# Performance work log

Hardware: AMD Instinct MI355X
Metric: run time of the kernel (lower is better)

## Reference

```python
import jax, jax.numpy as jnp
import numpy as np

DIM_VAL = 128
DIM_ATTN = 64

def setup_inputs() -> dict:
    key = jax.random.key(0)
    k_x, k_q, k_k, k_v = jax.random.split(key, 4)
    B, S = 4, 4096
    x = jax.random.normal(k_x, (B, S, DIM_VAL), dtype=jnp.float32)
    # nn.Linear(in, out, bias=False): weight shape [out, in]; y = x @ W^T
    Wq = jax.random.normal(k_q, (DIM_ATTN, DIM_VAL), dtype=jnp.float32) / np.sqrt(DIM_VAL)
    Wk = jax.random.normal(k_k, (DIM_ATTN, DIM_VAL), dtype=jnp.float32) / np.sqrt(DIM_VAL)
    Wv = jax.random.normal(k_v, (DIM_VAL, DIM_VAL), dtype=jnp.float32) / np.sqrt(DIM_VAL)
    return {"x": x, "Wq": Wq, "Wk": Wk, "Wv": Wv}

def reference(x, Wq, Wk, Wv):
    # QKV projections (bias-free linear: x @ W^T)
    Q = jnp.einsum('bsd,ad->bsa', x, Wq)   # [B,S,dim_attn]
    K = jnp.einsum('bsd,ad->bsa', x, Wk)   # [B,S,dim_attn]
    V = jnp.einsum('bsd,vd->bsv', x, Wv)   # [B,S,dim_val]
    scale = 1.0 / jnp.sqrt(jnp.asarray(Q.shape[-1], dtype=Q.dtype))
    scores = jnp.einsum('bqa,bka->bqk', Q, K) * scale  # [B,S,S]
    a = jax.nn.softmax(scores, axis=-1)
    return jnp.einsum('bqk,bkv->bqv', a, V)  # [B,S,dim_val]
```

## Files before the change

### kernel.cpp

```cpp
#include <hip/hip_runtime.h>

typedef _Float16 half8 __attribute__((ext_vector_type(8)));
typedef _Float16 half4v __attribute__((ext_vector_type(4)));
typedef float   float4v __attribute__((ext_vector_type(4)));

#define S_LEN 4096
#define NBATCH 4
#define NCHUNK 4
#define WS_W16 0
#define WS_QH  32768
#define WS_KH  1081344
#define WS_VT  2129920
#define WS_L   4227072
#define OACC_BYTE_OFF 8519680ull
#define OACC_F4_PER_CHUNK (NBATCH * S_LEN * 128 / 4)
#define LACC_BYTE_OFF (OACC_BYTE_OFF + (unsigned long long)NCHUNK * NBATCH * S_LEN * 128 * 4)
#define WS_NEED_BYTES (LACC_BYTE_OFF + (unsigned long long)NCHUNK * NBATCH * S_LEN * 4)

__global__ __launch_bounds__(256) void wcvt_kernel(const float* __restrict__ Wq,
                                                   const float* __restrict__ Wk,
                                                   const float* __restrict__ Wv,
                                                   _Float16* __restrict__ w16) {
    int i = blockIdx.x * 256 + threadIdx.x;
    int row = i >> 7, col = i & 127;
    float v;
    if (row < 64)       v = Wq[row * 128 + col];
    else if (row < 128) v = Wk[(row - 64) * 128 + col];
    else                v = Wv[(row - 128) * 128 + col];
    w16[i] = (_Float16)v;
}

__global__ __launch_bounds__(256) void zero_kernel(float4v* __restrict__ out4,
                                                   float4v* __restrict__ l4) {
    int i = blockIdx.x * 256 + threadIdx.x;
    out4[i] = (float4v){0.f, 0.f, 0.f, 0.f};
    if (i < 4096) l4[i] = (float4v){0.f, 0.f, 0.f, 0.f};
}

__global__ __launch_bounds__(256) void qkv_proj_kernel(const float* __restrict__ x,
                                                       const _Float16* __restrict__ w16,
                                                       _Float16* __restrict__ Qh,
                                                       _Float16* __restrict__ Kh,
                                                       _Float16* __restrict__ Vt) {
    __shared__ _Float16 xs[16 * 136];
    const int t = threadIdx.x;
    const int blk = blockIdx.x;
    const float* xb = x + (size_t)blk * 16 * 128;

    for (int it = 0; it < 2; ++it) {
        int i = t + it * 256;
        int row = i >> 5, c4 = i & 31;
        float4v f = ((const float4v*)xb)[i];
        half4v h;
        h[0] = (_Float16)f[0]; h[1] = (_Float16)f[1];
        h[2] = (_Float16)f[2]; h[3] = (_Float16)f[3];
        *(half4v*)&xs[row * 136 + c4 * 4] = h;
    }
    __syncthreads();

    const int w = t >> 6, lane = t & 63, quad = lane >> 4, n16 = lane & 15;

    half8 a[4];
    for (int c = 0; c < 4; ++c)
        a[c] = *(const half8*)&xs[n16 * 136 + c * 32 + quad * 8];

    float4v acc[4];
    for (int nb = 0; nb < 4; ++nb) acc[nb] = (float4v){0.f, 0.f, 0.f, 0.f};

    for (int c = 0; c < 4; ++c) {
        for (int nb = 0; nb < 4; ++nb) {
            int oc = w * 64 + nb * 16 + n16;
            half8 bfr = *(const half8*)&w16[(size_t)oc * 128 + c * 32 + quad * 8];
            acc[nb] = __builtin_amdgcn_mfma_f32_16x16x32_f16(a[c], bfr, acc[nb], 0, 0, 0);
        }
    }

    const int token0 = blk * 16 + quad * 4;
    if (w == 0) {
        for (int nb = 0; nb < 4; ++nb)
            for (int r = 0; r < 4; ++r)
                Qh[(size_t)(token0 + r) * 64 + nb * 16 + n16] = (_Float16)acc[nb][r];
    } else if (w == 1) {
        for (int nb = 0; nb < 4; ++nb)
            for (int r = 0; r < 4; ++r)
                Kh[(size_t)(token0 + r) * 64 + nb * 16 + n16] = (_Float16)acc[nb][r];
    } else {
        const int bb = token0 >> 12, s0 = token0 & 4095;
        const int kt = s0 >> 6, k0 = s0 & 63;
        const int grp = k0 >> 5, k32 = k0 & 31;
        const int g = k32 >> 4, q = (k32 >> 2) & 3;
        const int off = kt * 64 + grp * 32 + q * 8 + g * 4;
        for (int nb = 0; nb < 4; ++nb) {
            const int vc = (w - 2) * 64 + nb * 16 + n16;
            half4v h;
            h[0] = (_Float16)acc[nb][0]; h[1] = (_Float16)acc[nb][1];
            h[2] = (_Float16)acc[nb][2]; h[3] = (_Float16)acc[nb][3];
            *(half4v*)&Vt[((size_t)bb * 128 + vc) * S_LEN + off] = h;
        }
    }
}

#define KT 64
template <bool STAGED>
__global__ __launch_bounds__(256) void flash_kernel(const _Float16* __restrict__ Qh,
                                                    const _Float16* __restrict__ Kh,
                                                    const _Float16* __restrict__ Vt,
                                                    float* __restrict__ outp,
                                                    float* __restrict__ lp) {
    __shared__ _Float16 Ks[KT * 72];
    __shared__ _Float16 Vs[128 * 72];

    const int t = threadIdx.x;
    const int qt = blockIdx.x, chunk = blockIdx.y, b = blockIdx.z;
    const int w = t >> 6, lane = t & 63, quad = lane >> 4, n16 = lane & 15;

    const size_t qrowA = (size_t)b * S_LEN + qt * 128 + w * 16 + n16;
    const size_t qrowB = qrowA + 64;
    half8 aQ0A = *(const half8*)&Qh[qrowA * 64 + quad * 8];
    half8 aQ1A = *(const half8*)&Qh[qrowA * 64 + 32 + quad * 8];
    half8 aQ0B = *(const half8*)&Qh[qrowB * 64 + quad * 8];
    half8 aQ1B = *(const half8*)&Qh[qrowB * 64 + 32 + quad * 8];

    float4v OA[8], OB[8];
#pragma unroll
    for (int vb = 0; vb < 8; ++vb) {
        OA[vb] = (float4v){0.f, 0.f, 0.f, 0.f};
        OB[vb] = (float4v){0.f, 0.f, 0.f, 0.f};
    }
    float lsumA = 0.f, lsumB = 0.f;

    const _Float16* Kb = Kh + (size_t)b * S_LEN * 64;
    const _Float16* Vb = Vt + (size_t)b * 128 * S_LEN;

    const int kt0 = chunk * (S_LEN / KT / NCHUNK);
    const int kt1 = kt0 + (S_LEN / KT / NCHUNK);

    const int kr0 = t >> 3, kc0 = t & 7;
    const int kr1 = (t + 256) >> 3;

    half8 kreg0, kreg1, vreg[4];
    {
        const half8* srcK = (const half8*)(Kb + (size_t)kt0 * KT * 64);
        kreg0 = srcK[t];
        kreg1 = srcK[t + 256];
#pragma unroll
        for (int it = 0; it < 4; ++it) {
            int i = t + it * 256, row = i >> 3, c8 = i & 7;
            vreg[it] = *(const half8*)&Vb[(size_t)row * S_LEN + kt0 * KT + c8 * 8];
        }
    }

    for (int kt = kt0; kt < kt1; ++kt) {
        __syncthreads();
        *(half8*)&Ks[kr0 * 72 + kc0 * 8] = kreg0;
        *(half8*)&Ks[kr1 * 72 + kc0 * 8] = kreg1;
#pragma unroll
        for (int it = 0; it < 4; ++it) {
            int i = t + it * 256, row = i >> 3, c8 = i & 7;
            *(half8*)&Vs[row * 72 + c8 * 8] = vreg[it];
        }
        __syncthreads();

        if (kt + 1 < kt1) {
            const half8* srcK = (const half8*)(Kb + (size_t)(kt + 1) * KT * 64);
            kreg0 = srcK[t];
            kreg1 = srcK[t + 256];
#pragma unroll
            for (int it = 0; it < 4; ++it) {
                int i = t + it * 256, row = i >> 3, c8 = i & 7;
                vreg[it] = *(const half8*)&Vb[(size_t)row * S_LEN + (kt + 1) * KT + c8 * 8];
            }
        }

        half8 aP0A, aP1A, aP0B, aP1B;
        __builtin_amdgcn_s_setprio(1);
#pragma unroll
        for (int nb = 0; nb < 4; ++nb) {
            half8 bK0 = *(const half8*)&Ks[(nb * 16 + n16) * 72 + quad * 8];
            half8 bK1 = *(const half8*)&Ks[(nb * 16 + n16) * 72 + 32 + quad * 8];
            float4v scA = (float4v){0.f, 0.f, 0.f, 0.f};
            float4v scB = (float4v){0.f, 0.f, 0.f, 0.f};
            scA = __builtin_amdgcn_mfma_f32_16x16x32_f16(bK0, aQ0A, scA, 0, 0, 0);
            scA = __builtin_amdgcn_mfma_f32_16x16x32_f16(bK1, aQ1A, scA, 0, 0, 0);
            scB = __builtin_amdgcn_mfma_f32_16x16x32_f16(bK0, aQ0B, scB, 0, 0, 0);
            scB = __builtin_amdgcn_mfma_f32_16x16x32_f16(bK1, aQ1B, scB, 0, 0, 0);
#pragma unroll
            for (int r = 0; r < 4; ++r) {
                float pa = __builtin_amdgcn_exp2f(__builtin_fmaf(scA[r], 0.18033688f, -5.7707802f));
                lsumA += pa;
                float pb = __builtin_amdgcn_exp2f(__builtin_fmaf(scB[r], 0.18033688f, -5.7707802f));
                lsumB += pb;
                int slot = (nb & 1) * 4 + r;
                if (nb < 2) { aP0A[slot] = (_Float16)pa; aP0B[slot] = (_Float16)pb; }
                else        { aP1A[slot] = (_Float16)pa; aP1B[slot] = (_Float16)pb; }
            }
        }
        __builtin_amdgcn_s_setprio(0);

        __builtin_amdgcn_s_setprio(1);
#pragma unroll
        for (int vb = 0; vb < 8; ++vb) {
            const _Float16* vrow = &Vs[(vb * 16 + n16) * 72];
            half8 bV0 = *(const half8*)&vrow[quad * 8];
            half8 bV1 = *(const half8*)&vrow[32 + quad * 8];
            OA[vb] = __builtin_amdgcn_mfma_f32_16x16x32_f16(aP0A, bV0, OA[vb], 0, 0, 0);
            OA[vb] = __builtin_amdgcn_mfma_f32_16x16x32_f16(aP1A, bV1, OA[vb], 0, 0, 0);
            OB[vb] = __builtin_amdgcn_mfma_f32_16x16x32_f16(aP0B, bV0, OB[vb], 0, 0, 0);
            OB[vb] = __builtin_amdgcn_mfma_f32_16x16x32_f16(aP1B, bV1, OB[vb], 0, 0, 0);
        }
        __builtin_amdgcn_s_setprio(0);
    }

    lsumA += __shfl_xor(lsumA, 16);
    lsumA += __shfl_xor(lsumA, 32);
    lsumB += __shfl_xor(lsumB, 16);
    lsumB += __shfl_xor(lsumB, 32);

    const int rowbaseA = qt * 128 + w * 16;
    const int rowbaseB = rowbaseA + 64;
    const int row0A = rowbaseA + quad * 4;
    const int row0B = rowbaseB + quad * 4;

    if (STAGED) {
        const size_t cb = (size_t)chunk * NBATCH + b;
        if (quad == 0) {
            lp[cb * S_LEN + rowbaseA + n16] = lsumA;
            lp[cb * S_LEN + rowbaseB + n16] = lsumB;
        }
        float* obA = outp + (cb * S_LEN + row0A) * 128;
        float* obB = outp + (cb * S_LEN + row0B) * 128;
#pragma unroll
        for (int vb = 0; vb < 8; ++vb)
#pragma unroll
            for (int r = 0; r < 4; ++r) {
                obA[(size_t)r * 128 + vb * 16 + n16] = OA[vb][r];
                obB[(size_t)r * 128 + vb * 16 + n16] = OB[vb][r];
            }
    } else {
        if (quad == 0) {
            unsafeAtomicAdd(&lp[b * S_LEN + rowbaseA + n16], lsumA);
            unsafeAtomicAdd(&lp[b * S_LEN + rowbaseB + n16], lsumB);
        }
        float* obA = outp + ((size_t)b * S_LEN + row0A) * 128;
        float* obB = outp + ((size_t)b * S_LEN + row0B) * 128;
#pragma unroll
        for (int vb = 0; vb < 8; ++vb)
#pragma unroll
            for (int r = 0; r < 4; ++r) {
                unsafeAtomicAdd(&obA[(size_t)r * 128 + vb * 16 + n16], OA[vb][r]);
                unsafeAtomicAdd(&obB[(size_t)r * 128 + vb * 16 + n16], OB[vb][r]);
            }
    }
}

__global__ __launch_bounds__(256) void norm_sum_kernel(const float4v* __restrict__ oacc4,
                                                       const float* __restrict__ lacc,
                                                       float4v* __restrict__ out4) {
    int i = blockIdx.x * 256 + threadIdx.x;
    int row = i >> 5;
    float l = 0.f;
#pragma unroll
    for (int c = 0; c < NCHUNK; ++c) l += lacc[c * (NBATCH * S_LEN) + row];
    float4v s = (float4v){0.f, 0.f, 0.f, 0.f};
#pragma unroll
    for (int c = 0; c < NCHUNK; ++c) {
        float4v p = oacc4[(size_t)c * OACC_F4_PER_CHUNK + i];
        s[0] += p[0]; s[1] += p[1]; s[2] += p[2]; s[3] += p[3];
    }
    float inv = 1.0f / l;
    s[0] *= inv; s[1] *= inv; s[2] *= inv; s[3] *= inv;
    out4[i] = s;
}

__global__ __launch_bounds__(256) void norm_kernel(float4v* __restrict__ out4,
                                                   const float* __restrict__ lbuf) {
    int i = blockIdx.x * 256 + threadIdx.x;
    float inv = 1.0f / lbuf[i >> 5];
    float4v v = out4[i];
    v[0] *= inv; v[1] *= inv; v[2] *= inv; v[3] *= inv;
    out4[i] = v;
}

extern "C" void kernel_launch(void* const* d_in, const int* in_sizes, int n_in,
                              void* d_out, int out_size, void* d_ws, size_t ws_size,
                              hipStream_t stream) {
    const float* x  = (const float*)d_in[0];
    const float* Wq = (const float*)d_in[1];
    const float* Wk = (const float*)d_in[2];
    const float* Wv = (const float*)d_in[3];
    float* out = (float*)d_out;

    _Float16* ws = (_Float16*)d_ws;
    _Float16* w16 = ws + WS_W16;
    _Float16* Qh  = ws + WS_QH;
    _Float16* Kh  = ws + WS_KH;
    _Float16* Vt  = ws + WS_VT;
    float*    lbuf = (float*)(ws + WS_L);

    wcvt_kernel<<<128, 256, 0, stream>>>(Wq, Wk, Wv, w16);
    qkv_proj_kernel<<<NBATCH * S_LEN / 16, 256, 0, stream>>>(x, w16, Qh, Kh, Vt);

    if (ws_size >= (size_t)WS_NEED_BYTES) {
        float* oacc = (float*)((char*)d_ws + OACC_BYTE_OFF);
        float* lacc = (float*)((char*)d_ws + LACC_BYTE_OFF);
        flash_kernel<true><<<dim3(S_LEN / 128, NCHUNK, NBATCH), 256, 0, stream>>>(
            Qh, Kh, Vt, oacc, lacc);
        norm_sum_kernel<<<2048, 256, 0, stream>>>((const float4v*)oacc, lacc, (float4v*)out);
    } else {
        zero_kernel<<<2048, 256, 0, stream>>>((float4v*)out, (float4v*)lbuf);
        flash_kernel<false><<<dim3(S_LEN / 128, NCHUNK, NBATCH), 256, 0, stream>>>(
            Qh, Kh, Vt, out, lbuf);
        norm_kernel<<<2048, 256, 0, stream>>>((float4v*)out, lbuf);
    }
}
```

Measured before the change: 116.3 us.

## Double-buffer K/V tiles via direct global-to-LDS loads with XOR swizzle, fuse weight conversion

The flash kernel now stages K and V tiles straight from global memory into double-buffered LDS using global_load_lds, with an XOR swizzle replacing the padded layout to avoid bank conflicts. The prefetch of the next tile overlaps compute, and the loop drops one barrier and the register round-trip. Separately, the weight-conversion kernel is removed: the projection kernel reads fp32 weights and x directly and converts them in registers, saving a launch but re-reading weights per block. Doubling the LDS buffers may reduce occupancy.

```diff
diff --git a/kernel.cpp b/kernel.cpp
--- a/kernel.cpp
+++ b/kernel.cpp
@@ -7,7 +7,6 @@
 #define S_LEN 4096
 #define NBATCH 4
 #define NCHUNK 4
-#define WS_W16 0
 #define WS_QH  32768
 #define WS_KH  1081344
 #define WS_VT  2129920
@@ -17,17 +16,19 @@
 #define LACC_BYTE_OFF (OACC_BYTE_OFF + (unsigned long long)NCHUNK * NBATCH * S_LEN * 128 * 4)
 #define WS_NEED_BYTES (LACC_BYTE_OFF + (unsigned long long)NCHUNK * NBATCH * S_LEN * 4)
 
-__global__ __launch_bounds__(256) void wcvt_kernel(const float* __restrict__ Wq,
-                                                   const float* __restrict__ Wk,
-                                                   const float* __restrict__ Wv,
-                                                   _Float16* __restrict__ w16) {
-    int i = blockIdx.x * 256 + threadIdx.x;
-    int row = i >> 7, col = i & 127;
-    float v;
-    if (row < 64)       v = Wq[row * 128 + col];
-    else if (row < 128) v = Wk[(row - 64) * 128 + col];
-    else                v = Wv[(row - 128) * 128 + col];
-    w16[i] = (_Float16)v;
+static __device__ __forceinline__ half8 cvt8(float4v f0, float4v f1) {
+    half8 h;
+    h[0] = (_Float16)f0[0]; h[1] = (_Float16)f0[1];
+    h[2] = (_Float16)f0[2]; h[3] = (_Float16)f0[3];
+    h[4] = (_Float16)f1[0]; h[5] = (_Float16)f1[1];
+    h[6] = (_Float16)f1[2]; h[7] = (_Float16)f1[3];
+    return h;
+}
+
+static __device__ __forceinline__ void gload16(const _Float16* g, _Float16* l) {
+    __builtin_amdgcn_global_load_lds(
+        (const __attribute__((address_space(1))) void*)g,
+        (__attribute__((address_space(3))) void*)l, 16, 0, 0);
 }
 
 __global__ __launch_bounds__(256) void zero_kernel(float4v* __restrict__ out4,
@@ -38,42 +39,38 @@
 }
 
 __global__ __launch_bounds__(256) void qkv_proj_kernel(const float* __restrict__ x,
-                                                       const _Float16* __restrict__ w16,
+                                                       const float* __restrict__ Wq,
+                                                       const float* __restrict__ Wk,
+                                                       const float* __restrict__ Wv,
                                                        _Float16* __restrict__ Qh,
                                                        _Float16* __restrict__ Kh,
                                                        _Float16* __restrict__ Vt) {
-    __shared__ _Float16 xs[16 * 136];
-    const int t = threadIdx.x;
-    const int blk = blockIdx.x;
+    const int t = threadIdx.x, blk = blockIdx.x;
+    const int w = t >> 6, lane = t & 63, quad = lane >> 4, n16 = lane & 15;
     const float* xb = x + (size_t)blk * 16 * 128;
 
-    for (int it = 0; it < 2; ++it) {
-        int i = t + it * 256;
-        int row = i >> 5, c4 = i & 31;
-        float4v f = ((const float4v*)xb)[i];
-        half4v h;
-        h[0] = (_Float16)f[0]; h[1] = (_Float16)f[1];
-        h[2] = (_Float16)f[2]; h[3] = (_Float16)f[3];
-        *(half4v*)&xs[row * 136 + c4 * 4] = h;
-    }
-    __syncthreads();
-
-    const int w = t >> 6, lane = t & 63, quad = lane >> 4, n16 = lane & 15;
-
     half8 a[4];
+#pragma unroll
+    for (int c = 0; c < 4; ++c) {
+        const float* xr = xb + n16 * 128 + c * 32 + quad * 8;
+        a[c] = cvt8(*(const float4v*)xr, *(const float4v*)(xr + 4));
+    }
+
+    const float* Wsel = (w == 0) ? Wq : (w == 1) ? Wk : Wv;
+    const int rowoff = (w >= 2) ? (w - 2) * 64 : 0;
+
+    float4v acc[4];
+#pragma unroll
+    for (int nb = 0; nb < 4; ++nb) acc[nb] = (float4v){0.f, 0.f, 0.f, 0.f};
+
+#pragma unroll
     for (int c = 0; c < 4; ++c)
-        a[c] = *(const half8*)&xs[n16 * 136 + c * 32 + quad * 8];
-
-    float4v acc[4];
-    for (int nb = 0; nb < 4; ++nb) acc[nb] = (float4v){0.f, 0.f, 0.f, 0.f};
-
-    for (int c = 0; c < 4; ++c) {
+#pragma unroll
         for (int nb = 0; nb < 4; ++nb) {
-            int oc = w * 64 + nb * 16 + n16;
-            half8 bfr = *(const half8*)&w16[(size_t)oc * 128 + c * 32 + quad * 8];
+            const float* wr = Wsel + (size_t)(rowoff + nb * 16 + n16) * 128 + c * 32 + quad * 8;
+            half8 bfr = cvt8(*(const float4v*)wr, *(const float4v*)(wr + 4));
             acc[nb] = __builtin_amdgcn_mfma_f32_16x16x32_f16(a[c], bfr, acc[nb], 0, 0, 0);
         }
-    }
 
     const int token0 = blk * 16 + quad * 4;
     if (w == 0) {
@@ -107,12 +104,13 @@
                                                     const _Float16* __restrict__ Vt,
                                                     float* __restrict__ outp,
                                                     float* __restrict__ lp) {
-    __shared__ _Float16 Ks[KT * 72];
-    __shared__ _Float16 Vs[128 * 72];
+    __shared__ _Float16 Ks[2][KT * 64];
+    __shared__ _Float16 Vs[2][128 * 64];
 
     const int t = threadIdx.x;
     const int qt = blockIdx.x, chunk = blockIdx.y, b = blockIdx.z;
     const int w = t >> 6, lane = t & 63, quad = lane >> 4, n16 = lane & 15;
+    const int swz = n16 & 7;
 
     const size_t qrowA = (size_t)b * S_LEN + qt * 128 + w * 16 + n16;
     const size_t qrowB = qrowA + 64;
@@ -135,49 +133,39 @@
     const int kt0 = chunk * (S_LEN / KT / NCHUNK);
     const int kt1 = kt0 + (S_LEN / KT / NCHUNK);
 
-    const int kr0 = t >> 3, kc0 = t & 7;
-    const int kr1 = (t + 256) >> 3;
-
-    half8 kreg0, kreg1, vreg[4];
-    {
-        const half8* srcK = (const half8*)(Kb + (size_t)kt0 * KT * 64);
-        kreg0 = srcK[t];
-        kreg1 = srcK[t + 256];
-#pragma unroll
-        for (int it = 0; it < 4; ++it) {
-            int i = t + it * 256, row = i >> 3, c8 = i & 7;
-            vreg[it] = *(const half8*)&Vb[(size_t)row * S_LEN + kt0 * KT + c8 * 8];
-        }
-    }
-
+#define STAGE(bb, ktv) do {                                                    \
+        const _Float16* Ksrc = Kb + (size_t)(ktv) * KT * 64;                   \
+        _Float16* Kdst = &Ks[bb][0];                                           \
+        _Float16* Vdst = &Vs[bb][0];                                           \
+        for (int i_ = 0; i_ < 2; ++i_) {                                       \
+            int d_ = t + i_ * 256, row_ = d_ >> 3, ch_ = d_ & 7;               \
+            gload16(Ksrc + row_ * 64 + ((ch_ ^ (row_ & 7)) << 3), Kdst + d_ * 8); \
+        }                                                                      \
+        for (int i_ = 0; i_ < 4; ++i_) {                                       \
+            int d_ = t + i_ * 256, row_ = d_ >> 3, ch_ = d_ & 7;               \
+            gload16(Vb + (size_t)row_ * S_LEN + (ktv) * KT + ((ch_ ^ (row_ & 7)) << 3), \
+                    Vdst + d_ * 8);                                            \
+        }                                                                      \
+    } while (0)
+
+    STAGE(0, kt0);
+    asm volatile("s_waitcnt vmcnt(0)" ::: "memory");
+    __builtin_amdgcn_s_barrier();
+
+    int cur = 0;
     for (int kt = kt0; kt < kt1; ++kt) {
-        __syncthreads();
-        *(half8*)&Ks[kr0 * 72 + kc0 * 8] = kreg0;
-        *(half8*)&Ks[kr1 * 72 + kc0 * 8] = kreg1;
-#pragma unroll
-        for (int it = 0; it < 4; ++it) {
-            int i = t + it * 256, row = i >> 3, c8 = i & 7;
-            *(half8*)&Vs[row * 72 + c8 * 8] = vreg[it];
-        }
-        __syncthreads();
-
-        if (kt + 1 < kt1) {
-            const half8* srcK = (const half8*)(Kb + (size_t)(kt + 1) * KT * 64);
-            kreg0 = srcK[t];
-            kreg1 = srcK[t + 256];
-#pragma unroll
-            for (int it = 0; it < 4; ++it) {
-                int i = t + it * 256, row = i >> 3, c8 = i & 7;
-                vreg[it] = *(const half8*)&Vb[(size_t)row * S_LEN + (kt + 1) * KT + c8 * 8];
-            }
-        }
+        if (kt + 1 < kt1) STAGE(cur ^ 1, kt + 1);
+
+        const _Float16* Ksc = Ks[cur];
+        const _Float16* Vsc = Vs[cur];
 
         half8 aP0A, aP1A, aP0B, aP1B;
         __builtin_amdgcn_s_setprio(1);
 #pragma unroll
         for (int nb = 0; nb < 4; ++nb) {
-            half8 bK0 = *(const half8*)&Ks[(nb * 16 + n16) * 72 + quad * 8];
-            half8 bK1 = *(const half8*)&Ks[(nb * 16 + n16) * 72 + 32 + quad * 8];
+            const int krow = (nb * 16 + n16) * 64;
+            half8 bK0 = *(const half8*)&Ksc[krow + ((quad ^ swz) << 3)];
+            half8 bK1 = *(const half8*)&Ksc[krow + (((4 + quad) ^ swz) << 3)];
             float4v scA = (float4v){0.f, 0.f, 0.f, 0.f};
             float4v scB = (float4v){0.f, 0.f, 0.f, 0.f};
             scA = __builtin_amdgcn_mfma_f32_16x16x32_f16(bK0, aQ0A, scA, 0, 0, 0);
@@ -200,16 +188,23 @@
         __builtin_amdgcn_s_setprio(1);
 #pragma unroll
         for (int vb = 0; vb < 8; ++vb) {
-            const _Float16* vrow = &Vs[(vb * 16 + n16) * 72];
-            half8 bV0 = *(const half8*)&vrow[quad * 8];
-            half8 bV1 = *(const half8*)&vrow[32 + quad * 8];
+            const int vrow = (vb * 16 + n16) * 64;
+            half8 bV0 = *(const half8*)&Vsc[vrow + ((quad ^ swz) << 3)];
+            half8 bV1 = *(const half8*)&Vsc[vrow + (((4 + quad) ^ swz) << 3)];
             OA[vb] = __builtin_amdgcn_mfma_f32_16x16x32_f16(aP0A, bV0, OA[vb], 0, 0, 0);
             OA[vb] = __builtin_amdgcn_mfma_f32_16x16x32_f16(aP1A, bV1, OA[vb], 0, 0, 0);
             OB[vb] = __builtin_amdgcn_mfma_f32_16x16x32_f16(aP0B, bV0, OB[vb], 0, 0, 0);
             OB[vb] = __builtin_amdgcn_mfma_f32_16x16x32_f16(aP1B, bV1, OB[vb], 0, 0, 0);
         }
         __builtin_amdgcn_s_setprio(0);
-    }
+
+        if (kt + 1 < kt1) {
+            asm volatile("s_waitcnt vmcnt(0)" ::: "memory");
+            __builtin_amdgcn_s_barrier();
+            cur ^= 1;
+        }
+    }
+#undef STAGE
 
     lsumA += __shfl_xor(lsumA, 16);
     lsumA += __shfl_xor(lsumA, 32);
@@ -291,14 +286,12 @@
     float* out = (float*)d_out;
 
     _Float16* ws = (_Float16*)d_ws;
-    _Float16* w16 = ws + WS_W16;
     _Float16* Qh  = ws + WS_QH;
     _Float16* Kh  = ws + WS_KH;
     _Float16* Vt  = ws + WS_VT;
     float*    lbuf = (float*)(ws + WS_L);
 
-    wcvt_kernel<<<128, 256, 0, stream>>>(Wq, Wk, Wv, w16);
-    qkv_proj_kernel<<<NBATCH * S_LEN / 16, 256, 0, stream>>>(x, w16, Qh, Kh, Vt);
+    qkv_proj_kernel<<<NBATCH * S_LEN / 16, 256, 0, stream>>>(x, Wq, Wk, Wv, Qh, Kh, Vt);
 
     if (ws_size >= (size_t)WS_NEED_BYTES) {
         float* oacc = (float*)((char*)d_ws + OACC_BYTE_OFF);
```

New measurement: 124.7 us. +7.3%, slower.
